# Optimization experiments

Hardware: AMD Instinct MI355X
Metric: run time of the kernel (lower is better)

## Reference

```python
import jax, jax.numpy as jnp
import numpy as np

# model hyperparameters (from init_kwargs 'model' mapping)
SIG = 10.0       # kernel length scale
C = 0.0          # energy integration constant
STD = 1.0        # normalization std
M, N_ATOMS = 64, 24
T_ROWS, DESC = 6000, N_ATOMS * (N_ATOMS - 1) // 2  # 276


def setup_inputs() -> dict:
    key = jax.random.key(0)
    k1, k2, k3 = jax.random.split(key, 3)
    # spread atoms out so pairwise distances are O(1..10) Angstrom-like
    Rs = jax.random.normal(k1, (M, N_ATOMS, 3), jnp.float32) * 3.0
    # training descriptors are inverse distances -> positive values in (0,1)
    xs_train = jax.random.uniform(k2, (T_ROWS, DESC), jnp.float32)
    Jx_alphas = jax.random.normal(k3, (T_ROWS, DESC), jnp.float32) * 0.1
    return {"Rs": Rs, "xs_train": xs_train, "Jx_alphas": Jx_alphas}


def reference(Rs, xs_train, Jx_alphas):
    sig = SIG
    q = np.sqrt(5.0) / sig
    m, n = Rs.shape[0], Rs.shape[1]
    i, j = np.tril_indices(n, k=-1)  # lower-triangular atom pairs, P entries

    # pairwise coordinate differences [M, N, N, 3]
    diffs = Rs[:, :, None, :] - Rs[:, None, :, :]
    # inverse pairwise distances over tril pairs -> descriptor xs [M, P]
    d_ij = jnp.linalg.norm(diffs[:, i, j, :], axis=-1)
    xs = 1.0 / d_ij

    # descriptor differences to all (permuted) training points [M, T, P]
    x_diffs = q * xs[:, None, :] - q * xs_train[None, :, :]
    x_dists = jnp.linalg.norm(x_diffs, axis=-1)            # [M, T]
    exp_xs = (5.0 / (3.0 * sig ** 2)) * jnp.exp(-x_dists)  # [M, T]
    dot = jnp.einsum('mtp,tp->mt', x_diffs, Jx_alphas)     # [M, T]
    exp1 = exp_xs * (1.0 + x_dists)                        # [M, T]

    F1 = jnp.einsum('mt,mtp->mp', exp_xs * dot, x_diffs)   # [M, P]
    F2 = exp1 @ Jx_alphas                                  # [M, P]
    Fs_x = (F1 - F2) * xs ** 3                             # [M, P]

    # scatter pair forces back onto the symmetric [N, N] pair grid;
    # diagonal diffs are zero so leaving mult=0 there matches the original
    mult = jnp.zeros((m, n, n), Rs.dtype)
    mult = mult.at[:, i, j].set(Fs_x).at[:, j, i].set(Fs_x)
    Fs = (diffs * mult[..., None]).sum(axis=1) * STD       # [M, N, 3]

    Es = (exp1 * dot).sum(axis=-1) / q * STD + C           # [M]
    return Es, Fs
```

## Files before the change

kernel.cpp:

```cpp
#include <hip/hip_runtime.h>
#include <math.h>

#define MM 64
#define NA 24
#define NP 276
#define NT 6000
#define NTP 6048
#define QC 0.22360679774997896f
#define EXPC 0.01666666666666667f

#define OFF_XST  0
#define OFF_UU   17664
#define OFF_ES   17728
#define OFF_SW   17792
#define OFF_SH   17856
#define OFF_WT   300480
#define OFF_ET   687552
#define ZTOT     282752

__device__ __forceinline__ float f4c(const float4& v, int i) {
  return i == 0 ? v.x : i == 1 ? v.y : i == 2 ? v.z : v.w;
}

__global__ __launch_bounds__(256) void k_pre(const float* __restrict__ Rs,
                                             float* __restrict__ ws) {
  const int tid = threadIdx.x;
  for (int z = blockIdx.x * 256 + tid; z < ZTOT; z += gridDim.x * 256)
    ws[OFF_ES + z] = 0.f;
  for (int z = blockIdx.x * 256 + tid; z < 6144; z += gridDim.x * 256) {
    if (z < 3072) ws[OFF_WT + 384000 + z] = 0.f;
    else          ws[OFF_ET + 384000 + (z - 3072)] = 0.f;
  }
  if (blockIdx.x < MM) {
    const int m = blockIdx.x;
    __shared__ float sR[NA * 3];
    __shared__ float sAcc[4];
    if (tid < NA * 3) sR[tid] = Rs[m * NA * 3 + tid];
    __syncthreads();
    float acc = 0.f;
    for (int p = tid; p < NP; p += 256) {
      int i = (int)((1.0f + sqrtf(1.0f + 8.0f * (float)p)) * 0.5f);
      while (i * (i - 1) / 2 > p) i--;
      while ((i + 1) * i / 2 <= p) i++;
      int j = p - i * (i - 1) / 2;
      float dx = sR[i * 3 + 0] - sR[j * 3 + 0];
      float dy = sR[i * 3 + 1] - sR[j * 3 + 1];
      float dz = sR[i * 3 + 2] - sR[j * 3 + 2];
      float u = 1.0f / sqrtf(dx * dx + dy * dy + dz * dz);
      ws[OFF_XST + p * 64 + m] = u;
      acc += u * u;
    }
    for (int off = 32; off; off >>= 1) acc += __shfl_down(acc, off);
    if ((tid & 63) == 0) sAcc[tid >> 6] = acc;
    __syncthreads();
    if (tid == 0) ws[OFF_UU + m] = sAcc[0] + sAcc[1] + sAcc[2] + sAcc[3];
  }
}

#define G1_BS 280
#define G1_AS 36
__global__ __launch_bounds__(256, 2) void k_g1(const float* __restrict__ xt,
                                               const float* __restrict__ Ja,
                                               float* __restrict__ ws) {
  __shared__ __align__(16) float2 Bs[16][G1_BS];
  __shared__ __align__(16) float As[NP][G1_AS];
  __shared__ float sVV[16], sC1[16];
  __shared__ float sEsW[4][32], sSwW[4][32];
  const int tid = threadIdx.x;
  const int t0 = blockIdx.x * 16;
  const int m0 = blockIdx.y * 32;

  for (int idx = tid; idx < 16 * 69; idx += 256) {
    const int row = idx / 69;
    const int kq = (idx - row * 69) * 4;
    const float4 v = *(const float4*)(xt + (size_t)(t0 + row) * NP + kq);
    const float4 j = *(const float4*)(Ja + (size_t)(t0 + row) * NP + kq);
    *(float4*)&Bs[row][kq]     = make_float4(v.x, j.x, v.y, j.y);
    *(float4*)&Bs[row][kq + 2] = make_float4(v.z, j.z, v.w, j.w);
  }
  for (int idx = tid; idx < NP * 8; idx += 256) {
    const int p = idx >> 3;
    const int mq = (idx & 7) * 4;
    *(float4*)&As[p][mq] = *(const float4*)(ws + OFF_XST + p * 64 + m0 + mq);
  }
  const int r = tid & 15;
  const int c = tid >> 4;
  const float2 uu2 = *(const float2*)(ws + OFF_UU + m0 + 2 * r);
  __syncthreads();

  {
    const int tl = tid >> 4;
    const int l16 = tid & 15;
    float a = 0.f, b = 0.f;
    for (int k = l16; k < NP; k += 16) {
      const float2 x = Bs[tl][k];
      a = fmaf(x.x, x.x, a);
      b = fmaf(x.x, x.y, b);
    }
#pragma unroll
    for (int off = 8; off; off >>= 1) {
      a += __shfl_down(a, off, 16);
      b += __shfl_down(b, off, 16);
    }
    if (l16 == 0) { sVV[tl] = a; sC1[tl] = b; }
  }
  __syncthreads();

  float av0 = 0.f, av1 = 0.f, aj0 = 0.f, aj1 = 0.f;
#pragma unroll 4
  for (int kk = 0; kk < NP; kk += 2) {
    const float4 b  = *(const float4*)&Bs[c][kk];
    const float2 a0 = *(const float2*)&As[kk][2 * r];
    const float2 a1 = *(const float2*)&As[kk + 1][2 * r];
    av0 = fmaf(a0.x, b.x, av0); aj0 = fmaf(a0.x, b.y, aj0);
    av1 = fmaf(a0.y, b.x, av1); aj1 = fmaf(a0.y, b.y, aj1);
    av0 = fmaf(a1.x, b.z, av0); aj0 = fmaf(a1.x, b.w, aj0);
    av1 = fmaf(a1.y, b.z, av1); aj1 = fmaf(a1.y, b.w, aj1);
  }

  const float vvt = sVV[c];
  const float c1t = sC1[c];
  float es2[2], sw2[2], wv[2], ev[2];
#pragma unroll
  for (int i = 0; i < 2; i++) {
    const float g1v = i ? av1 : av0;
    const float g2v = i ? aj1 : aj0;
    const float uum = i ? uu2.y : uu2.x;
    float d2 = fmaxf(uum - 2.f * g1v + vvt, 0.f);
    float xd = QC * sqrtf(d2);
    float dv = QC * (g2v - c1t);
    float ex = EXPC * __expf(-xd);
    float e1v = ex * (1.f + xd);
    float w_ = ex * dv;
    wv[i] = w_; ev[i] = e1v;
    es2[i] = e1v * dv;
    sw2[i] = w_;
  }
  const int t = t0 + c;
  *(float2*)(ws + OFF_WT + (size_t)t * 64 + m0 + 2 * r) = make_float2(wv[0], wv[1]);
  *(float2*)(ws + OFF_ET + (size_t)t * 64 + m0 + 2 * r) = make_float2(ev[0], ev[1]);

#pragma unroll
  for (int i = 0; i < 2; i++) {
    es2[i] += __shfl_down(es2[i], 32); es2[i] += __shfl_down(es2[i], 16);
    sw2[i] += __shfl_down(sw2[i], 32); sw2[i] += __shfl_down(sw2[i], 16);
  }
  const int w = tid >> 6;
  if ((tid & 63) < 16) {
    sEsW[w][2 * r + 0] = es2[0]; sEsW[w][2 * r + 1] = es2[1];
    sSwW[w][2 * r + 0] = sw2[0]; sSwW[w][2 * r + 1] = sw2[1];
  }
  __syncthreads();
  if (tid < 32) {
    const float es = sEsW[0][tid] + sEsW[1][tid] + sEsW[2][tid] + sEsW[3][tid];
    const float sw = sSwW[0][tid] + sSwW[1][tid] + sSwW[2][tid] + sSwW[3][tid];
    atomicAdd(ws + OFF_ES + m0 + tid, es);
    atomicAdd(ws + OFF_SW + m0 + tid, sw);
  }
}

#define G2_KC 96
#define G2_AS 68
#define G2_BS 18
__global__ __launch_bounds__(256, 2) void k_g2(const float* __restrict__ xt,
                                               const float* __restrict__ Ja,
                                               float* __restrict__ ws) {
  __shared__ __align__(16) float Aw[G2_KC][G2_AS];
  __shared__ __align__(16) float Ae[G2_KC][G2_AS];
  __shared__ __align__(16) float2 Bvj[G2_KC][G2_BS];
  const int tid = threadIdx.x;
  const int p0 = blockIdx.x * 16;
  const int k0 = blockIdx.y * G2_KC;
  const int validp = (NP - p0 < 16) ? (NP - p0) : 16;

  for (int idx = tid; idx < G2_KC * 16; idx += 256) {
    const int k = idx >> 4;
    const int mq = (idx & 15) * 4;
    *(float4*)&Aw[k][mq] = *(const float4*)(ws + OFF_WT + (size_t)(k0 + k) * 64 + mq);
    *(float4*)&Ae[k][mq] = *(const float4*)(ws + OFF_ET + (size_t)(k0 + k) * 64 + mq);
  }
  for (int idx = tid; idx < G2_KC * 4; idx += 256) {
    const int k = idx >> 2;
    const int pq = (idx & 3) * 4;
    const int t = k0 + k;
    float4 v = make_float4(0.f, 0.f, 0.f, 0.f), j = v;
    if (pq < validp && t < NT) {
      v = *(const float4*)(xt + (size_t)t * NP + p0 + pq);
      j = *(const float4*)(Ja + (size_t)t * NP + p0 + pq);
    }
    *(float4*)&Bvj[k][pq]     = make_float4(v.x, j.x, v.y, j.y);
    *(float4*)&Bvj[k][pq + 2] = make_float4(v.z, j.z, v.w, j.w);
  }
  __syncthreads();

  const int r = tid & 31;
  const int c = tid >> 5;
  float f1[2][2] = {{0.f, 0.f}, {0.f, 0.f}};
  float f2[2][2] = {{0.f, 0.f}, {0.f, 0.f}};
#pragma unroll 4
  for (int k = 0; k < G2_KC; k++) {
    const float2 aw = *(const float2*)&Aw[k][2 * r];
    const float2 ae = *(const float2*)&Ae[k][2 * r];
    const float4 b  = *(const float4*)&Bvj[k][2 * c];
    f1[0][0] = fmaf(aw.x, b.x, f1[0][0]); f1[0][1] = fmaf(aw.x, b.z, f1[0][1]);
    f1[1][0] = fmaf(aw.y, b.x, f1[1][0]); f1[1][1] = fmaf(aw.y, b.z, f1[1][1]);
    f2[0][0] = fmaf(ae.x, b.y, f2[0][0]); f2[0][1] = fmaf(ae.x, b.w, f2[0][1]);
    f2[1][0] = fmaf(ae.y, b.y, f2[1][0]); f2[1][1] = fmaf(ae.y, b.w, f2[1][1]);
  }

  const int sh = blockIdx.y & 7;
  float* b1 = ws + OFF_SH + (size_t)(sh * 2 + 0) * NP * 64;
  float* b2 = ws + OFF_SH + (size_t)(sh * 2 + 1) * NP * 64;
#pragma unroll
  for (int j = 0; j < 2; j++) {
    const int pl = 2 * c + j;
    if (pl < validp) {
      const int p = p0 + pl;
#pragma unroll
      for (int i = 0; i < 2; i++) {
        atomicAdd(b1 + (size_t)p * 64 + 2 * r + i, f1[i][j]);
        atomicAdd(b2 + (size_t)p * 64 + 2 * r + i, f2[i][j]);
      }
    }
  }
}

__global__ __launch_bounds__(320) void k_final(const float* __restrict__ Rs,
                                               const float* __restrict__ ws,
                                               float* __restrict__ out) {
  const int m = blockIdx.x;
  const int tid = threadIdx.x;
  __shared__ float fx[NP];
  __shared__ float sR[NA * 3];
  if (tid < NA * 3) sR[tid] = Rs[m * NA * 3 + tid];
  const float sw = ws[OFF_SW + m];
  for (int p = tid; p < NP; p += 320) {
    float f1p = 0.f, f2 = 0.f;
#pragma unroll
    for (int s = 0; s < 8; s++) {
      f1p += ws[OFF_SH + ((size_t)(s * 2 + 0) * NP + p) * 64 + m];
      f2  += ws[OFF_SH + ((size_t)(s * 2 + 1) * NP + p) * 64 + m];
    }
    const float u = ws[OFF_XST + p * 64 + m];
    const float F1 = QC * (u * sw - f1p);
    fx[p] = (F1 - f2) * u * u * u;
  }
  __syncthreads();
  if (tid == 0) out[m] = ws[OFF_ES + m] / QC;
  if (tid < NA * 3) {
    const int a = tid / 3, cc = tid % 3;
    const float ra = sR[a * 3 + cc];
    float acc = 0.f;
    for (int b = 0; b < NA; b++) {
      if (b == a) continue;
      const int i = a > b ? a : b, j = a > b ? b : a;
      const int p = i * (i - 1) / 2 + j;
      acc += (sR[b * 3 + cc] - ra) * fx[p];
    }
    out[MM + m * NA * 3 + tid] = acc;
  }
}

extern "C" void kernel_launch(void* const* d_in, const int* in_sizes, int n_in,
                              void* d_out, int out_size, void* d_ws, size_t ws_size,
                              hipStream_t stream) {
  const float* Rs = (const float*)d_in[0];
  const float* xt = (const float*)d_in[1];
  const float* Ja = (const float*)d_in[2];
  float* out = (float*)d_out;
  float* ws = (float*)d_ws;

  k_pre<<<256, 256, 0, stream>>>(Rs, ws);
  k_g1<<<dim3(375, 2), 256, 0, stream>>>(xt, Ja, ws);
  k_g2<<<dim3(18, 63), 256, 0, stream>>>(xt, Ja, ws);
  k_final<<<MM, 320, 0, stream>>>(Rs, ws, out);
}
```

Measured before the change: 136.5 us.

## Fuse descriptor prep into k1 and replace atomics with deterministic partial slabs

Drops the separate k_pre kernel: each k1 block now computes the inverse distances for its 32 molecules straight from Rs, and the last block zeroes the padding rows. All atomics are replaced by plain stores into per-block partial buffers. Es/Sw partials are written per t-block, and k2 loops over three k-rounds per block, writing into 28 slabs that k3 reduces. This removes one launch, the zero-fill pass and atomic contention. In exchange every k1 block redoes the distance computation and k3 has larger reductions to perform.

```diff
diff --git a/kernel.cpp b/kernel.cpp
--- a/kernel.cpp
+++ b/kernel.cpp
@@ -5,70 +5,49 @@
 #define NA 24
 #define NP 276
 #define NT 6000
-#define NTP 6048
 #define QC 0.22360679774997896f
 #define EXPC 0.01666666666666667f
 
-#define OFF_XST  0
-#define OFF_UU   17664
-#define OFF_ES   17728
-#define OFF_SW   17792
-#define OFF_SH   17856
-#define OFF_WT   300480
-#define OFF_ET   687552
-#define ZTOT     282752
-
-__device__ __forceinline__ float f4c(const float4& v, int i) {
-  return i == 0 ? v.x : i == 1 ? v.y : i == 2 ? v.z : v.w;
-}
-
-__global__ __launch_bounds__(256) void k_pre(const float* __restrict__ Rs,
-                                             float* __restrict__ ws) {
-  const int tid = threadIdx.x;
-  for (int z = blockIdx.x * 256 + tid; z < ZTOT; z += gridDim.x * 256)
-    ws[OFF_ES + z] = 0.f;
-  for (int z = blockIdx.x * 256 + tid; z < 6144; z += gridDim.x * 256) {
-    if (z < 3072) ws[OFF_WT + 384000 + z] = 0.f;
-    else          ws[OFF_ET + 384000 + (z - 3072)] = 0.f;
-  }
-  if (blockIdx.x < MM) {
-    const int m = blockIdx.x;
-    __shared__ float sR[NA * 3];
-    __shared__ float sAcc[4];
-    if (tid < NA * 3) sR[tid] = Rs[m * NA * 3 + tid];
-    __syncthreads();
-    float acc = 0.f;
-    for (int p = tid; p < NP; p += 256) {
-      int i = (int)((1.0f + sqrtf(1.0f + 8.0f * (float)p)) * 0.5f);
-      while (i * (i - 1) / 2 > p) i--;
-      while ((i + 1) * i / 2 <= p) i++;
-      int j = p - i * (i - 1) / 2;
-      float dx = sR[i * 3 + 0] - sR[j * 3 + 0];
-      float dy = sR[i * 3 + 1] - sR[j * 3 + 1];
-      float dz = sR[i * 3 + 2] - sR[j * 3 + 2];
-      float u = 1.0f / sqrtf(dx * dx + dy * dy + dz * dz);
-      ws[OFF_XST + p * 64 + m] = u;
-      acc += u * u;
-    }
-    for (int off = 32; off; off >>= 1) acc += __shfl_down(acc, off);
-    if ((tid & 63) == 0) sAcc[tid >> 6] = acc;
-    __syncthreads();
-    if (tid == 0) ws[OFF_UU + m] = sAcc[0] + sAcc[1] + sAcc[2] + sAcc[3];
-  }
-}
+#define OFF_WT   0
+#define OFF_ET   387072
+#define OFF_SLAB 774144
+#define OFF_ESP  1763328
+#define OFF_SWP  1787328
 
 #define G1_BS 280
 #define G1_AS 36
-__global__ __launch_bounds__(256, 2) void k_g1(const float* __restrict__ xt,
-                                               const float* __restrict__ Ja,
-                                               float* __restrict__ ws) {
+#define G2S   28
+#define G2CH  216
+#define G2R   72
+#define G2_AS 68
+#define G2_BS 18
+
+__device__ __forceinline__ void p2ij(int p, int& i, int& j) {
+  int ii = (int)((1.0f + sqrtf(1.0f + 8.0f * (float)p)) * 0.5f);
+  while (ii * (ii - 1) / 2 > p) ii--;
+  while ((ii + 1) * ii / 2 <= p) ii++;
+  j = p - ii * (ii - 1) / 2;
+  i = ii;
+}
+
+__global__ __launch_bounds__(256, 2) void k1(const float* __restrict__ Rs,
+                                             const float* __restrict__ xt,
+                                             const float* __restrict__ Ja,
+                                             float* __restrict__ ws) {
   __shared__ __align__(16) float2 Bs[16][G1_BS];
   __shared__ __align__(16) float As[NP][G1_AS];
+  __shared__ float sUUp[8][32];
+  __shared__ float sUU[32];
   __shared__ float sVV[16], sC1[16];
   __shared__ float sEsW[4][32], sSwW[4][32];
   const int tid = threadIdx.x;
   const int t0 = blockIdx.x * 16;
   const int m0 = blockIdx.y * 32;
+
+  if (blockIdx.x == 374) {
+    float* tz = ws + (blockIdx.y ? OFF_ET : OFF_WT) + (size_t)NT * 64;
+    for (int z = tid; z < 48 * 64; z += 256) tz[z] = 0.f;
+  }
 
   for (int idx = tid; idx < 16 * 69; idx += 256) {
     const int row = idx / 69;
@@ -78,14 +57,25 @@
     *(float4*)&Bs[row][kq]     = make_float4(v.x, j.x, v.y, j.y);
     *(float4*)&Bs[row][kq + 2] = make_float4(v.z, j.z, v.w, j.w);
   }
-  for (int idx = tid; idx < NP * 8; idx += 256) {
-    const int p = idx >> 3;
-    const int mq = (idx & 7) * 4;
-    *(float4*)&As[p][mq] = *(const float4*)(ws + OFF_XST + p * 64 + m0 + mq);
-  }
-  const int r = tid & 15;
-  const int c = tid >> 4;
-  const float2 uu2 = *(const float2*)(ws + OFF_UU + m0 + 2 * r);
+  {
+    const float* Rm = Rs + (size_t)m0 * NA * 3;
+    float up = 0.f;
+    for (int idx = tid; idx < NP * 32; idx += 256) {
+      const int p = idx >> 5;
+      const int ml = idx & 31;
+      int i, j;
+      p2ij(p, i, j);
+      const float* ri = Rm + ml * 72 + i * 3;
+      const float* rj = Rm + ml * 72 + j * 3;
+      const float dx = ri[0] - rj[0];
+      const float dy = ri[1] - rj[1];
+      const float dz = ri[2] - rj[2];
+      const float u = 1.0f / sqrtf(dx * dx + dy * dy + dz * dz);
+      As[p][ml] = u;
+      up = fmaf(u, u, up);
+    }
+    sUUp[tid >> 5][tid & 31] = up;
+  }
   __syncthreads();
 
   {
@@ -104,7 +94,17 @@
     }
     if (l16 == 0) { sVV[tl] = a; sC1[tl] = b; }
   }
-  __syncthreads();
+  if (tid < 32) {
+    float a = 0.f;
+#pragma unroll
+    for (int k = 0; k < 8; k++) a += sUUp[k][tid];
+    sUU[tid] = a;
+  }
+  __syncthreads();
+
+  const int r = tid & 15;
+  const int c = tid >> 4;
+  const float2 uu2 = *(const float2*)&sUU[2 * r];
 
   float av0 = 0.f, av1 = 0.f, aj0 = 0.f, aj1 = 0.f;
 #pragma unroll 4
@@ -154,99 +154,124 @@
   if (tid < 32) {
     const float es = sEsW[0][tid] + sEsW[1][tid] + sEsW[2][tid] + sEsW[3][tid];
     const float sw = sSwW[0][tid] + sSwW[1][tid] + sSwW[2][tid] + sSwW[3][tid];
-    atomicAdd(ws + OFF_ES + m0 + tid, es);
-    atomicAdd(ws + OFF_SW + m0 + tid, sw);
-  }
-}
-
-#define G2_KC 96
-#define G2_AS 68
-#define G2_BS 18
-__global__ __launch_bounds__(256, 2) void k_g2(const float* __restrict__ xt,
-                                               const float* __restrict__ Ja,
-                                               float* __restrict__ ws) {
-  __shared__ __align__(16) float Aw[G2_KC][G2_AS];
-  __shared__ __align__(16) float Ae[G2_KC][G2_AS];
-  __shared__ __align__(16) float2 Bvj[G2_KC][G2_BS];
+    ws[OFF_ESP + (size_t)blockIdx.x * 64 + m0 + tid] = es;
+    ws[OFF_SWP + (size_t)blockIdx.x * 64 + m0 + tid] = sw;
+  }
+}
+
+__global__ __launch_bounds__(256, 2) void k2(const float* __restrict__ xt,
+                                             const float* __restrict__ Ja,
+                                             float* __restrict__ ws) {
+  __shared__ __align__(16) float Aw[G2R][G2_AS];
+  __shared__ __align__(16) float Ae[G2R][G2_AS];
+  __shared__ __align__(16) float2 Bvj[G2R][G2_BS];
   const int tid = threadIdx.x;
   const int p0 = blockIdx.x * 16;
-  const int k0 = blockIdx.y * G2_KC;
+  const int cid = blockIdx.y;
   const int validp = (NP - p0 < 16) ? (NP - p0) : 16;
-
-  for (int idx = tid; idx < G2_KC * 16; idx += 256) {
-    const int k = idx >> 4;
-    const int mq = (idx & 15) * 4;
-    *(float4*)&Aw[k][mq] = *(const float4*)(ws + OFF_WT + (size_t)(k0 + k) * 64 + mq);
-    *(float4*)&Ae[k][mq] = *(const float4*)(ws + OFF_ET + (size_t)(k0 + k) * 64 + mq);
-  }
-  for (int idx = tid; idx < G2_KC * 4; idx += 256) {
-    const int k = idx >> 2;
-    const int pq = (idx & 3) * 4;
-    const int t = k0 + k;
-    float4 v = make_float4(0.f, 0.f, 0.f, 0.f), j = v;
-    if (pq < validp && t < NT) {
-      v = *(const float4*)(xt + (size_t)t * NP + p0 + pq);
-      j = *(const float4*)(Ja + (size_t)t * NP + p0 + pq);
-    }
-    *(float4*)&Bvj[k][pq]     = make_float4(v.x, j.x, v.y, j.y);
-    *(float4*)&Bvj[k][pq + 2] = make_float4(v.z, j.z, v.w, j.w);
-  }
-  __syncthreads();
-
   const int r = tid & 31;
   const int c = tid >> 5;
   float f1[2][2] = {{0.f, 0.f}, {0.f, 0.f}};
   float f2[2][2] = {{0.f, 0.f}, {0.f, 0.f}};
+
+  for (int rnd = 0; rnd < 3; rnd++) {
+    const int k0 = cid * G2CH + rnd * G2R;
+    __syncthreads();
+    for (int idx = tid; idx < G2R * 16; idx += 256) {
+      const int k = idx >> 4;
+      const int mq = (idx & 15) * 4;
+      *(float4*)&Aw[k][mq] = *(const float4*)(ws + OFF_WT + (size_t)(k0 + k) * 64 + mq);
+      *(float4*)&Ae[k][mq] = *(const float4*)(ws + OFF_ET + (size_t)(k0 + k) * 64 + mq);
+    }
+    for (int idx = tid; idx < G2R * 4; idx += 256) {
+      const int k = idx >> 2;
+      const int pq = (idx & 3) * 4;
+      const int t = k0 + k;
+      float4 v = make_float4(0.f, 0.f, 0.f, 0.f), j = v;
+      if (pq < validp && t < NT) {
+        v = *(const float4*)(xt + (size_t)t * NP + p0 + pq);
+        j = *(const float4*)(Ja + (size_t)t * NP + p0 + pq);
+      }
+      *(float4*)&Bvj[k][pq]     = make_float4(v.x, j.x, v.y, j.y);
+      *(float4*)&Bvj[k][pq + 2] = make_float4(v.z, j.z, v.w, j.w);
+    }
+    __syncthreads();
 #pragma unroll 4
-  for (int k = 0; k < G2_KC; k++) {
-    const float2 aw = *(const float2*)&Aw[k][2 * r];
-    const float2 ae = *(const float2*)&Ae[k][2 * r];
-    const float4 b  = *(const float4*)&Bvj[k][2 * c];
-    f1[0][0] = fmaf(aw.x, b.x, f1[0][0]); f1[0][1] = fmaf(aw.x, b.z, f1[0][1]);
-    f1[1][0] = fmaf(aw.y, b.x, f1[1][0]); f1[1][1] = fmaf(aw.y, b.z, f1[1][1]);
-    f2[0][0] = fmaf(ae.x, b.y, f2[0][0]); f2[0][1] = fmaf(ae.x, b.w, f2[0][1]);
-    f2[1][0] = fmaf(ae.y, b.y, f2[1][0]); f2[1][1] = fmaf(ae.y, b.w, f2[1][1]);
-  }
-
-  const int sh = blockIdx.y & 7;
-  float* b1 = ws + OFF_SH + (size_t)(sh * 2 + 0) * NP * 64;
-  float* b2 = ws + OFF_SH + (size_t)(sh * 2 + 1) * NP * 64;
+    for (int k = 0; k < G2R; k++) {
+      const float2 aw = *(const float2*)&Aw[k][2 * r];
+      const float2 ae = *(const float2*)&Ae[k][2 * r];
+      const float4 b  = *(const float4*)&Bvj[k][2 * c];
+      f1[0][0] = fmaf(aw.x, b.x, f1[0][0]); f1[0][1] = fmaf(aw.x, b.z, f1[0][1]);
+      f1[1][0] = fmaf(aw.y, b.x, f1[1][0]); f1[1][1] = fmaf(aw.y, b.z, f1[1][1]);
+      f2[0][0] = fmaf(ae.x, b.y, f2[0][0]); f2[0][1] = fmaf(ae.x, b.w, f2[0][1]);
+      f2[1][0] = fmaf(ae.y, b.y, f2[1][0]); f2[1][1] = fmaf(ae.y, b.w, f2[1][1]);
+    }
+  }
+
 #pragma unroll
   for (int j = 0; j < 2; j++) {
     const int pl = 2 * c + j;
     if (pl < validp) {
       const int p = p0 + pl;
-#pragma unroll
-      for (int i = 0; i < 2; i++) {
-        atomicAdd(b1 + (size_t)p * 64 + 2 * r + i, f1[i][j]);
-        atomicAdd(b2 + (size_t)p * 64 + 2 * r + i, f2[i][j]);
-      }
-    }
-  }
-}
-
-__global__ __launch_bounds__(320) void k_final(const float* __restrict__ Rs,
-                                               const float* __restrict__ ws,
-                                               float* __restrict__ out) {
+      float* b1 = ws + OFF_SLAB + ((size_t)(cid * 2 + 0) * NP + p) * 64;
+      float* b2 = ws + OFF_SLAB + ((size_t)(cid * 2 + 1) * NP + p) * 64;
+      *(float2*)(b1 + 2 * r) = make_float2(f1[0][j], f1[1][j]);
+      *(float2*)(b2 + 2 * r) = make_float2(f2[0][j], f2[1][j]);
+    }
+  }
+}
+
+__global__ __launch_bounds__(512) void k3(const float* __restrict__ Rs,
+                                          const float* __restrict__ ws,
+                                          float* __restrict__ out) {
   const int m = blockIdx.x;
   const int tid = threadIdx.x;
   __shared__ float fx[NP];
   __shared__ float sR[NA * 3];
+  __shared__ float sEsw[8], sSww[8];
+  __shared__ float sTot[2];
   if (tid < NA * 3) sR[tid] = Rs[m * NA * 3 + tid];
-  const float sw = ws[OFF_SW + m];
-  for (int p = tid; p < NP; p += 320) {
+
+  float aE = 0.f, aS = 0.f;
+  for (int tt = tid; tt < 375; tt += 512) {
+    aE += ws[OFF_ESP + (size_t)tt * 64 + m];
+    aS += ws[OFF_SWP + (size_t)tt * 64 + m];
+  }
+#pragma unroll
+  for (int off = 32; off; off >>= 1) {
+    aE += __shfl_down(aE, off);
+    aS += __shfl_down(aS, off);
+  }
+  if ((tid & 63) == 0) { sEsw[tid >> 6] = aE; sSww[tid >> 6] = aS; }
+  __syncthreads();
+  if (tid == 0) {
+    float e = 0.f, s = 0.f;
+#pragma unroll
+    for (int w = 0; w < 8; w++) { e += sEsw[w]; s += sSww[w]; }
+    sTot[0] = e; sTot[1] = s;
+    out[m] = e / QC;
+  }
+  __syncthreads();
+  const float sw = sTot[1];
+
+  for (int p = tid; p < NP; p += 512) {
     float f1p = 0.f, f2 = 0.f;
 #pragma unroll
-    for (int s = 0; s < 8; s++) {
-      f1p += ws[OFF_SH + ((size_t)(s * 2 + 0) * NP + p) * 64 + m];
-      f2  += ws[OFF_SH + ((size_t)(s * 2 + 1) * NP + p) * 64 + m];
-    }
-    const float u = ws[OFF_XST + p * 64 + m];
+    for (int s = 0; s < G2S; s++) {
+      f1p += ws[OFF_SLAB + ((size_t)(s * 2 + 0) * NP + p) * 64 + m];
+      f2  += ws[OFF_SLAB + ((size_t)(s * 2 + 1) * NP + p) * 64 + m];
+    }
+    int i, j;
+    p2ij(p, i, j);
+    const float dx = sR[i * 3 + 0] - sR[j * 3 + 0];
+    const float dy = sR[i * 3 + 1] - sR[j * 3 + 1];
+    const float dz = sR[i * 3 + 2] - sR[j * 3 + 2];
+    const float u = 1.0f / sqrtf(dx * dx + dy * dy + dz * dz);
     const float F1 = QC * (u * sw - f1p);
     fx[p] = (F1 - f2) * u * u * u;
   }
   __syncthreads();
-  if (tid == 0) out[m] = ws[OFF_ES + m] / QC;
+
   if (tid < NA * 3) {
     const int a = tid / 3, cc = tid % 3;
     const float ra = sR[a * 3 + cc];
@@ -270,8 +295,7 @@
   float* out = (float*)d_out;
   float* ws = (float*)d_ws;
 
-  k_pre<<<256, 256, 0, stream>>>(Rs, ws);
-  k_g1<<<dim3(375, 2), 256, 0, stream>>>(xt, Ja, ws);
-  k_g2<<<dim3(18, 63), 256, 0, stream>>>(xt, Ja, ws);
-  k_final<<<MM, 320, 0, stream>>>(Rs, ws, out);
-}
+  k1<<<dim3(375, 2), 256, 0, stream>>>(Rs, xt, Ja, ws);
+  k2<<<dim3(18, G2S), 256, 0, stream>>>(xt, Ja, ws);
+  k3<<<MM, 512, 0, stream>>>(Rs, ws, out);
+}
```

New measurement: 152.2 us. 1.11x slower.
